# Optimization experiments

Hardware: AMD Instinct MI355X
Metric: run time of the kernel (lower is better)

## Reference

```python
import jax, jax.numpy as jnp
import numpy as np

D_MODEL = 1024
N_HEADS = 16
D_HEAD = D_MODEL // N_HEADS          # 64
FRACTION_TO_ROTATE = 0.25
ROT_DIM = int(FRACTION_TO_ROTATE * D_HEAD)  # 16 (even)
ROPE_BASE = 10000.0


def setup_inputs() -> dict:
    key = jax.random.key(0)
    ks = jax.random.split(key, 10)
    B, S = 2, 2048
    init = lambda k, fan_in, shape: jax.random.normal(k, shape, jnp.float32) / np.sqrt(fan_in)
    return {
        "x": jax.random.normal(ks[0], (B, S, D_MODEL), jnp.float32),
        "Wq": init(ks[1], D_MODEL, (D_MODEL, D_MODEL)),
        "bq": jnp.zeros((D_MODEL,), jnp.float32),
        "Wk": init(ks[2], D_MODEL, (D_MODEL, D_MODEL)),
        "bk": jnp.zeros((D_MODEL,), jnp.float32),
        "Wv": init(ks[3], D_MODEL, (D_MODEL, D_MODEL)),
        "bv": jnp.zeros((D_MODEL,), jnp.float32),
        "Wo": init(ks[4], D_MODEL, (D_MODEL, D_MODEL)),
        "bo": jnp.zeros((D_MODEL,), jnp.float32),
    }


def _apply_partial_rope(t, cos, sin):
    # t: [B, H, S, d_head]; rotate first ROT_DIM dims, pass the rest through.
    rot, rest = t[..., :ROT_DIM], t[..., ROT_DIM:]
    half = ROT_DIM // 2
    t1, t2 = rot[..., :half], rot[..., half:]
    # cos/sin: [S, half] -> broadcast over [B, H]
    r1 = t1 * cos - t2 * sin
    r2 = t1 * sin + t2 * cos
    return jnp.concatenate([r1, r2, rest], axis=-1)


def reference(x, Wq, bq, Wk, bk, Wv, bv, Wo, bo):
    B, S, D = x.shape
    q = (x @ Wq + bq).reshape(B, S, N_HEADS, D_HEAD).transpose(0, 2, 1, 3)
    k = (x @ Wk + bk).reshape(B, S, N_HEADS, D_HEAD).transpose(0, 2, 1, 3)
    v = (x @ Wv + bv).reshape(B, S, N_HEADS, D_HEAD).transpose(0, 2, 1, 3)

    half = ROT_DIM // 2
    inv_freq = 1.0 / (ROPE_BASE ** (jnp.arange(half, dtype=jnp.float32) / half))
    angles = jnp.arange(S, dtype=jnp.float32)[:, None] * inv_freq  # [S, half]
    cos, sin = jnp.cos(angles), jnp.sin(angles)

    q = _apply_partial_rope(q, cos, sin)
    k = _apply_partial_rope(k, cos, sin)

    scale = 1.0 / np.sqrt(D_HEAD).astype(np.float32)
    scores = jnp.einsum("bhqd,bhkd->bhqk", q, k) * scale  # [B,H,S,S]
    causal = jnp.tril(jnp.ones((S, S), dtype=bool))
    scores = jnp.where(causal, scores, jnp.finfo(scores.dtype).min)
    probs = jax.nn.softmax(scores, axis=-1)

    out = jnp.einsum("bhqk,bhkd->bhqd", probs, v)  # [B,H,S,d_head]
    out = out.transpose(0, 2, 1, 3).reshape(B, S, D)
    return out @ Wo + bo
```

## Files before the change

kernel.cpp:

```cpp
#include <hip/hip_runtime.h>
#include <hip/hip_bf16.h>
#include <math.h>

constexpr int DM = 1024;
constexpr int SEQ = 2048;
constexpr int BATCH = 2;
constexpr int NH = 16;
constexpr int DH = 64;
constexpr int MROWS = BATCH * SEQ;
constexpr float SCALE = 0.125f;

typedef __attribute__((ext_vector_type(8))) short short8;
typedef __attribute__((ext_vector_type(4))) float f32x4;
typedef unsigned short ushort_t;

__device__ __forceinline__ unsigned short f2b(float f) {
    __hip_bfloat16 h = __float2bfloat16(f);
    return __builtin_bit_cast(unsigned short, h);
}
__device__ __forceinline__ float b2f(unsigned short u) {
    unsigned int t = ((unsigned int)u) << 16;
    return __builtin_bit_cast(float, t);
}
__device__ __forceinline__ unsigned int cvtpk_bf16(float lo, float hi) {
    unsigned int r;
    asm("v_cvt_pk_bf16_f32 %0, %1, %2" : "=v"(r) : "v"(lo), "v"(hi));
    return r;
}
__device__ __forceinline__ f32x4 mfma16_bf16(uint2 a, uint2 b, f32x4 c) {
    asm volatile("v_mfma_f32_16x16x16_bf16 %0, %1, %2, %0"
                 : "+v"(c) : "v"(a), "v"(b));
    return c;
}

__device__ __forceinline__ void gload16(const ushort_t* g, ushort_t* l) {
    __builtin_amdgcn_global_load_lds(
        (const __attribute__((address_space(1))) void*)g,
        (__attribute__((address_space(3))) void*)l, 16, 0, 0);
}

__global__ __launch_bounds__(256) void conv_x(const float* __restrict__ x,
                                              ushort_t* __restrict__ xb) {
    const size_t idx = (size_t)blockIdx.x * 256 + threadIdx.x;
    const float4* src = (const float4*)(x + idx * 8);
    float4 a = src[0], b = src[1];
    short8 v;
    v[0] = (short)f2b(a.x); v[1] = (short)f2b(a.y);
    v[2] = (short)f2b(a.z); v[3] = (short)f2b(a.w);
    v[4] = (short)f2b(b.x); v[5] = (short)f2b(b.y);
    v[6] = (short)f2b(b.z); v[7] = (short)f2b(b.w);
    *(short8*)(xb + idx * 8) = v;
}

__global__ __launch_bounds__(256) void conv_w(
    const float* __restrict__ Wq, const float* __restrict__ Wk,
    const float* __restrict__ Wv, const float* __restrict__ Wo,
    ushort_t* __restrict__ Wqt, ushort_t* __restrict__ Wkt,
    ushort_t* __restrict__ Wvt, ushort_t* __restrict__ Wot) {
    const float* W; ushort_t* Wt;
    switch (blockIdx.z) {
        case 0:  W = Wq; Wt = Wqt; break;
        case 1:  W = Wk; Wt = Wkt; break;
        case 2:  W = Wv; Wt = Wvt; break;
        default: W = Wo; Wt = Wot; break;
    }
    __shared__ float L[64][65];
    const int n0 = blockIdx.x * 64, k0 = blockIdx.y * 64;
    const int t = threadIdx.x;
    const int tr = t >> 4, tc4 = (t & 15) * 4;
#pragma unroll
    for (int i = 0; i < 4; ++i) {
        int kk = tr + i * 16;
        float4 v = *(const float4*)&W[(size_t)(k0 + kk) * DM + n0 + tc4];
        L[kk][tc4 + 0] = v.x; L[kk][tc4 + 1] = v.y;
        L[kk][tc4 + 2] = v.z; L[kk][tc4 + 3] = v.w;
    }
    __syncthreads();
#pragma unroll
    for (int i = 0; i < 4; ++i) {
        int nn = tr + i * 16;
        ushort4 u;
        u.x = f2b(L[tc4 + 0][nn]); u.y = f2b(L[tc4 + 1][nn]);
        u.z = f2b(L[tc4 + 2][nn]); u.w = f2b(L[tc4 + 3][nn]);
        *(ushort4*)&Wt[(size_t)(n0 + nn) * DM + k0 + tc4] = u;
    }
}

#define BM 128
#define BN 128
#define BKK 32
#define NKT (DM / BKK)

__device__ __forceinline__ void stage_tile(const ushort_t* __restrict__ A,
                                           const ushort_t* __restrict__ B,
                                           int row0, int col0, int kt,
                                           ushort_t* As, ushort_t* Bs, int tid) {
#pragma unroll
    for (int i = 0; i < 2; ++i) {
        int f = i * 256 + tid;
        int r = f >> 2, c = (f & 3) ^ (r & 3);
        gload16(&A[(size_t)(row0 + r) * DM + kt * BKK + c * 8], &As[f * 8]);
        gload16(&B[(size_t)(col0 + r) * DM + kt * BKK + c * 8], &Bs[f * 8]);
    }
}

__device__ __forceinline__ void mfma_core(const ushort_t* __restrict__ A,
                                          const ushort_t* __restrict__ B,
                                          int row0, int col0,
                                          ushort_t* smem, f32x4 (&acc)[4][4]) {
    const int tid = threadIdx.x;
    const int wave = tid >> 6, lane = tid & 63;
    const int lg = lane >> 4, ln = lane & 15;
    const int wr = wave >> 1, wc = wave & 1;

    stage_tile(A, B, row0, col0, 0, smem, smem + 4096, tid);
    __syncthreads();

    int cur = 0;
    for (int kt = 0; kt < NKT; ++kt) {
        ushort_t* As = smem + cur * 8192;
        ushort_t* Bs = As + 4096;
        if (kt + 1 < NKT) {
            ushort_t* An = smem + (cur ^ 1) * 8192;
            stage_tile(A, B, row0, col0, kt + 1, An, An + 4096, tid);
        }

        short8 af[4], bf[4];
#pragma unroll
        for (int mi = 0; mi < 4; ++mi) {
            int r = wr * 64 + mi * 16 + ln;
            af[mi] = *(const short8*)&As[r * 32 + ((lg ^ (r & 3)) * 8)];
        }
#pragma unroll
        for (int ni = 0; ni < 4; ++ni) {
            int r = wc * 64 + ni * 16 + ln;
            bf[ni] = *(const short8*)&Bs[r * 32 + ((lg ^ (r & 3)) * 8)];
        }
        __builtin_amdgcn_s_setprio(1);
#pragma unroll
        for (int mi = 0; mi < 4; ++mi)
#pragma unroll
            for (int ni = 0; ni < 4; ++ni)
                acc[mi][ni] = __builtin_amdgcn_mfma_f32_16x16x32_bf16(
                    af[mi], bf[ni], acc[mi][ni], 0, 0, 0);
        __builtin_amdgcn_s_setprio(0);

        __syncthreads();
        cur ^= 1;
    }
}

__global__ __launch_bounds__(256) void mfma_gemm_qkv(
    const ushort_t* __restrict__ xb,
    const ushort_t* __restrict__ Wqt, const ushort_t* __restrict__ Wkt,
    const ushort_t* __restrict__ Wvt,
    const float* __restrict__ bq, const float* __restrict__ bk,
    const float* __restrict__ bv,
    ushort_t* __restrict__ qb, ushort_t* __restrict__ kb,
    ushort_t* __restrict__ vtb) {
    const ushort_t* W; const float* bias;
    if (blockIdx.z == 0)      { W = Wqt; bias = bq; }
    else if (blockIdx.z == 1) { W = Wkt; bias = bk; }
    else                      { W = Wvt; bias = bv; }

    const int row0 = blockIdx.y * BM;
    const int col0 = blockIdx.x * BN;
    __shared__ ushort_t smem[16384];
    f32x4 acc[4][4] = {};
    mfma_core(xb, W, row0, col0, smem, acc);

    const int tid = threadIdx.x;
    const int wave = tid >> 6, lane = tid & 63;
    const int lg = lane >> 4, ln = lane & 15;
    const int wr = wave >> 1, wc = wave & 1;
    const bool isV = (blockIdx.z == 2);

    __syncthreads();
    ushort_t* Cs = smem;
#pragma unroll
    for (int mi = 0; mi < 4; ++mi)
#pragma unroll
        for (int ni = 0; ni < 4; ++ni)
#pragma unroll
            for (int r = 0; r < 4; ++r) {
                int mrel = wr * 64 + mi * 16 + lg * 4 + r;
                int nrel = wc * 64 + ni * 16 + ln;
                float v = acc[mi][ni][r] + bias[col0 + nrel];
                Cs[isV ? (nrel * 128 + mrel) : (mrel * 128 + nrel)] = f2b(v);
            }
    __syncthreads();

    if (!isV) {
        ushort_t* out = (blockIdx.z == 0) ? qb : kb;
#pragma unroll
        for (int i = 0; i < 8; ++i) {
            int f = i * 256 + tid;
            int rrow = f >> 4, c8 = f & 15;
            int m = row0 + rrow;
            int b = m >> 11, s = m & (SEQ - 1);
            int n = col0 + c8 * 8;
            int h = n >> 6, d = n & 63;
            short8 val;
            if (d < 16) {
                const ushort_t* base = &Cs[rrow * 128 + (c8 & 8) * 8];
                const bool hi = (d >= 8);
#pragma unroll
                for (int j = 0; j < 8; ++j) {
                    float t1 = b2f(base[j]);
                    float t2 = b2f(base[8 + j]);
                    float invf = __expf(-(float)j * 1.1512925465f);
                    float ang = (float)s * invf;
                    float c_, si_;
                    __sincosf(ang, &si_, &c_);
                    val[j] = (short)f2b(hi ? (t1 * si_ + t2 * c_)
                                           : (t1 * c_ - t2 * si_));
                }
            } else {
                val = *(const short8*)&Cs[rrow * 128 + c8 * 8];
            }
            *(short8*)&out[((size_t)((b * NH + h) * SEQ) + s) * DH + d] = val;
        }
    } else {
#pragma unroll
        for (int i = 0; i < 8; ++i) {
            int f = i * 256 + tid;
            int nrow = f >> 4, c8 = f & 15;
            int n = col0 + nrow;
            int h = n >> 6, d = n & 63;
            int m = row0 + c8 * 8;
            int b = m >> 11, s = m & (SEQ - 1);
            *(short8*)&vtb[((size_t)((b * NH + h) * DH) + d) * SEQ + s] =
                *(const short8*)&Cs[nrow * 128 + c8 * 8];
        }
    }
}

__global__ __launch_bounds__(256) void mfma_gemm_out(
    const ushort_t* __restrict__ ctxb, const ushort_t* __restrict__ Wot,
    const float* __restrict__ bo, float* __restrict__ out) {
    const int row0 = blockIdx.y * BM;
    const int col0 = blockIdx.x * BN;
    __shared__ ushort_t smem[16384];
    f32x4 acc[4][4] = {};
    mfma_core(ctxb, Wot, row0, col0, smem, acc);

    const int tid = threadIdx.x;
    const int wave = tid >> 6, lane = tid & 63;
    const int lg = lane >> 4, ln = lane & 15;
    const int wr = wave >> 1, wc = wave & 1;
#pragma unroll
    for (int mi = 0; mi < 4; ++mi)
#pragma unroll
        for (int ni = 0; ni < 4; ++ni)
#pragma unroll
            for (int r = 0; r < 4; ++r) {
                int m = row0 + wr * 64 + mi * 16 + lg * 4 + r;
                int n = col0 + wc * 64 + ni * 16 + ln;
                out[(size_t)m * DM + n] = acc[mi][ni][r] + bo[n];
            }
}

#define AQT 64
#define AKT 64
#define NQT (SEQ / AQT)

__global__ __launch_bounds__(256) void attn_mfma(
    const ushort_t* __restrict__ qb, const ushort_t* __restrict__ kb,
    const ushort_t* __restrict__ vtb, ushort_t* __restrict__ ctxb) {
    constexpr float C1 = 0.18033688f;
    constexpr float M2 = 1.44269504f;
    const int bh = blockIdx.x;
    const int y = blockIdx.y;
    const int y0 = y & 7, g = y >> 3;
    const int qt = (g == 0) ? y0 : (g == 1) ? (15 - y0)
                 : (g == 2) ? (16 + y0) : (31 - y0);
    const int q0 = qt * AQT;

    const int tid = threadIdx.x;
    const int wave = tid >> 6;
    const int lane = tid & 63;
    const int lg = lane >> 4;
    const int ln = lane & 15;

    __shared__ ushort_t KT[2][64 * 64];
    __shared__ ushort_t VT[2][64 * 64];

    const ushort_t* kbase = kb + (size_t)bh * SEQ * DH;
    const ushort_t* vbase = vtb + (size_t)bh * DH * SEQ;
    const int b = bh >> 4, h = bh & 15;

    const ushort_t* qrow = qb + ((size_t)bh * SEQ + q0 + wave * 16 + ln) * DH;
    short8 qf0 = *(const short8*)&qrow[lg * 8];
    short8 qf1 = *(const short8*)&qrow[32 + lg * 8];

    f32x4 o[4];
#pragma unroll
    for (int nt = 0; nt < 4; nt++) o[nt] = f32x4{0.f, 0.f, 0.f, 0.f};
    float l = 0.f;

    const int ntiles = qt + 1;

#pragma unroll
    for (int i = 0; i < 2; i++) {
        int f = i * 256 + tid;
        int r = f >> 3, p = f & 7, c = p ^ (r & 7);
        gload16(&kbase[(size_t)r * DH + c * 8], &KT[0][f * 8]);
        gload16(&vbase[(size_t)r * SEQ + c * 8], &VT[0][f * 8]);
    }

    int cur = 0;
    for (int t = 0; t < ntiles; ++t) {
        __syncthreads();

        if (t + 1 < ntiles) {
            const int nb0 = (t + 1) * AKT;
            const int nxt = cur ^ 1;
#pragma unroll
            for (int i = 0; i < 2; i++) {
                int f = i * 256 + tid;
                int r = f >> 3, p = f & 7, c = p ^ (r & 7);
                gload16(&kbase[(size_t)(nb0 + r) * DH + c * 8], &KT[nxt][f * 8]);
                gload16(&vbase[(size_t)r * SEQ + nb0 + c * 8], &VT[nxt][f * 8]);
            }
        }

        float st[4][4];
        __builtin_amdgcn_s_setprio(1);
#pragma unroll
        for (int kt = 0; kt < 4; kt++) {
            f32x4 acc = f32x4{0.f, 0.f, 0.f, 0.f};
            int krow = kt * 16 + ln;
            short8 b0 = *(const short8*)&KT[cur][krow * 64 + ((lg ^ (krow & 7)) * 8)];
            short8 b1 = *(const short8*)&KT[cur][krow * 64 + (((4 + lg) ^ (krow & 7)) * 8)];
            acc = __builtin_amdgcn_mfma_f32_16x16x32_bf16(b0, qf0, acc, 0, 0, 0);
            acc = __builtin_amdgcn_mfma_f32_16x16x32_bf16(b1, qf1, acc, 0, 0, 0);
#pragma unroll
            for (int r = 0; r < 4; r++) st[kt][r] = acc[r];
        }
        __builtin_amdgcn_s_setprio(0);

        if (t == ntiles - 1) {
            const int qrel = wave * 16 + ln;
#pragma unroll
            for (int kt = 0; kt < 4; kt++)
#pragma unroll
                for (int r = 0; r < 4; r++)
                    if (kt * 16 + lg * 4 + r > qrel) st[kt][r] = -1e30f;
        }

        uint2 pkq[4];
#pragma unroll
        for (int kt = 0; kt < 4; kt++) {
            float pv[4];
#pragma unroll
            for (int r = 0; r < 4; r++) {
                pv[r] = exp2f(fmaf(C1, st[kt][r], -M2));
                l += pv[r];
            }
            pkq[kt].x = cvtpk_bf16(pv[0], pv[1]);
            pkq[kt].y = cvtpk_bf16(pv[2], pv[3]);
        }

        __builtin_amdgcn_s_setprio(1);
#pragma unroll
        for (int nt = 0; nt < 4; nt++) {
            int vrow = nt * 16 + ln;
#pragma unroll
            for (int kt = 0; kt < 4; kt++) {
                int chunk = (2 * kt + (lg >> 1)) ^ (vrow & 7);
                uint2 vb = *(const uint2*)&VT[cur][vrow * 64 + chunk * 8 + (lg & 1) * 4];
                o[nt] = mfma16_bf16(pkq[kt], vb, o[nt]);
            }
        }
        __builtin_amdgcn_s_setprio(0);

        cur ^= 1;
    }

    l += __shfl_xor(l, 16);
    l += __shfl_xor(l, 32);
    const float rcp = 1.f / l;
#pragma unroll
    for (int r = 0; r < 4; r++) {
        float invl = __shfl(rcp, (lane & 48) | (lg * 4 + r));
        int qg = q0 + wave * 16 + lg * 4 + r;
        ushort_t* op = ctxb + ((size_t)(b * SEQ + qg)) * DM + h * DH;
#pragma unroll
        for (int nt = 0; nt < 4; nt++)
            op[nt * 16 + ln] = f2b(o[nt][r] * invl);
    }
}

extern "C" void kernel_launch(void* const* d_in, const int* in_sizes, int n_in,
                              void* d_out, int out_size, void* d_ws, size_t ws_size,
                              hipStream_t stream) {
    const float* x  = (const float*)d_in[0];
    const float* Wq = (const float*)d_in[1];
    const float* bq = (const float*)d_in[2];
    const float* Wk = (const float*)d_in[3];
    const float* bk = (const float*)d_in[4];
    const float* Wv = (const float*)d_in[5];
    const float* bv = (const float*)d_in[6];
    const float* Wo = (const float*)d_in[7];
    const float* bo = (const float*)d_in[8];
    float* out = (float*)d_out;

    constexpr size_t TSZ = (size_t)MROWS * DM;
    constexpr size_t WSZ = (size_t)DM * DM;
    ushort_t* xb  = (ushort_t*)d_ws;
    ushort_t* Wqt = xb + TSZ;
    ushort_t* Wkt = Wqt + WSZ;
    ushort_t* Wvt = Wkt + WSZ;
    ushort_t* Wot = Wvt + WSZ;
    ushort_t* qbp = Wot + WSZ;
    ushort_t* kbp = qbp + TSZ;
    ushort_t* vtp = kbp + TSZ;
    ushort_t* ctxb = vtp + TSZ;

    conv_x<<<TSZ / 8 / 256, 256, 0, stream>>>(x, xb);
    conv_w<<<dim3(16, 16, 4), 256, 0, stream>>>(Wq, Wk, Wv, Wo, Wqt, Wkt, Wvt, Wot);

    mfma_gemm_qkv<<<dim3(DM / BN, MROWS / BM, 3), 256, 0, stream>>>(
        xb, Wqt, Wkt, Wvt, bq, bk, bv, qbp, kbp, vtp);

    attn_mfma<<<dim3(BATCH * NH, NQT), 256, 0, stream>>>(qbp, kbp, vtp, ctxb);

    mfma_gemm_out<<<dim3(DM / BN, MROWS / BM), 256, 0, stream>>>(ctxb, Wot, bo, out);
}
```

Baseline: 120.8 us.

## Split long causal attention query tiles into two KV chunks with a reduce kernel

Query tiles 16-31 are split into two blocks, one covering KV tiles 0-15 and one covering the rest, so long causal rows no longer sit on a single block. Each split writes unnormalized bf16 partial outputs and row sums into reused workspace, and a new reduce kernel adds them and normalizes. This is meant to balance work across blocks and cut the tail of the attention grid. The cost is an extra launch, extra memory traffic and bf16 rounding of the partials. The asm volatile on the MFMA is also dropped so the compiler can schedule it more freely.

```diff
diff --git a/kernel.cpp b/kernel.cpp
--- a/kernel.cpp
+++ b/kernel.cpp
@@ -28,8 +28,8 @@
     return r;
 }
 __device__ __forceinline__ f32x4 mfma16_bf16(uint2 a, uint2 b, f32x4 c) {
-    asm volatile("v_mfma_f32_16x16x16_bf16 %0, %1, %2, %0"
-                 : "+v"(c) : "v"(a), "v"(b));
+    asm("v_mfma_f32_16x16x16_bf16 %0, %1, %2, %0"
+        : "+v"(c) : "v"(a), "v"(b));
     return c;
 }
 
@@ -266,14 +266,17 @@
 
 __global__ __launch_bounds__(256) void attn_mfma(
     const ushort_t* __restrict__ qb, const ushort_t* __restrict__ kb,
-    const ushort_t* __restrict__ vtb, ushort_t* __restrict__ ctxb) {
+    const ushort_t* __restrict__ vtb, ushort_t* __restrict__ ctxb,
+    ushort_t* __restrict__ opart, float* __restrict__ lpart) {
     constexpr float C1 = 0.18033688f;
     constexpr float M2 = 1.44269504f;
     const int bh = blockIdx.x;
     const int y = blockIdx.y;
-    const int y0 = y & 7, g = y >> 3;
-    const int qt = (g == 0) ? y0 : (g == 1) ? (15 - y0)
-                 : (g == 2) ? (16 + y0) : (31 - y0);
+
+    int qt, t0, t1, chunk;
+    if (y < 16)      { qt = 16 + y;  t0 = 0;  t1 = 16;     chunk = 0; }
+    else if (y < 32) { qt = 47 - y;  t0 = 16; t1 = qt + 1; chunk = 1; }
+    else             { qt = 47 - y;  t0 = 0;  t1 = qt + 1; chunk = -1; }
     const int q0 = qt * AQT;
 
     const int tid = threadIdx.x;
@@ -298,21 +301,19 @@
     for (int nt = 0; nt < 4; nt++) o[nt] = f32x4{0.f, 0.f, 0.f, 0.f};
     float l = 0.f;
 
-    const int ntiles = qt + 1;
-
 #pragma unroll
     for (int i = 0; i < 2; i++) {
         int f = i * 256 + tid;
         int r = f >> 3, p = f & 7, c = p ^ (r & 7);
-        gload16(&kbase[(size_t)r * DH + c * 8], &KT[0][f * 8]);
-        gload16(&vbase[(size_t)r * SEQ + c * 8], &VT[0][f * 8]);
+        gload16(&kbase[(size_t)(t0 * AKT + r) * DH + c * 8], &KT[0][f * 8]);
+        gload16(&vbase[(size_t)r * SEQ + t0 * AKT + c * 8], &VT[0][f * 8]);
     }
 
     int cur = 0;
-    for (int t = 0; t < ntiles; ++t) {
+    for (int t = t0; t < t1; ++t) {
         __syncthreads();
 
-        if (t + 1 < ntiles) {
+        if (t + 1 < t1) {
             const int nb0 = (t + 1) * AKT;
             const int nxt = cur ^ 1;
 #pragma unroll
@@ -339,7 +340,7 @@
         }
         __builtin_amdgcn_s_setprio(0);
 
-        if (t == ntiles - 1) {
+        if (t == qt) {
             const int qrel = wave * 16 + ln;
 #pragma unroll
             for (int kt = 0; kt < 4; kt++)
@@ -367,8 +368,8 @@
             int vrow = nt * 16 + ln;
 #pragma unroll
             for (int kt = 0; kt < 4; kt++) {
-                int chunk = (2 * kt + (lg >> 1)) ^ (vrow & 7);
-                uint2 vb = *(const uint2*)&VT[cur][vrow * 64 + chunk * 8 + (lg & 1) * 4];
+                int chunk16 = (2 * kt + (lg >> 1)) ^ (vrow & 7);
+                uint2 vb = *(const uint2*)&VT[cur][vrow * 64 + chunk16 * 8 + (lg & 1) * 4];
                 o[nt] = mfma16_bf16(pkq[kt], vb, o[nt]);
             }
         }
@@ -379,15 +380,58 @@
 
     l += __shfl_xor(l, 16);
     l += __shfl_xor(l, 32);
-    const float rcp = 1.f / l;
-#pragma unroll
-    for (int r = 0; r < 4; r++) {
-        float invl = __shfl(rcp, (lane & 48) | (lg * 4 + r));
-        int qg = q0 + wave * 16 + lg * 4 + r;
-        ushort_t* op = ctxb + ((size_t)(b * SEQ + qg)) * DM + h * DH;
-#pragma unroll
-        for (int nt = 0; nt < 4; nt++)
-            op[nt * 16 + ln] = f2b(o[nt][r] * invl);
+
+    if (chunk >= 0) {
+        const int pid = ((bh << 4) + (qt - 16)) * 2 + chunk;
+        if (lg == 0) lpart[pid * 64 + wave * 16 + ln] = l;
+        ushort_t* ob = opart + (size_t)pid * 4096;
+#pragma unroll
+        for (int r = 0; r < 4; r++) {
+            int qrel = wave * 16 + lg * 4 + r;
+#pragma unroll
+            for (int nt = 0; nt < 4; nt++)
+                ob[qrel * 64 + nt * 16 + ln] = f2b(o[nt][r]);
+        }
+    } else {
+        const float rcp = 1.f / l;
+#pragma unroll
+        for (int r = 0; r < 4; r++) {
+            float invl = __shfl(rcp, (lane & 48) | (lg * 4 + r));
+            int qg = q0 + wave * 16 + lg * 4 + r;
+            ushort_t* op = ctxb + ((size_t)(b * SEQ + qg)) * DM + h * DH;
+#pragma unroll
+            for (int nt = 0; nt < 4; nt++)
+                op[nt * 16 + ln] = f2b(o[nt][r] * invl);
+        }
+    }
+}
+
+__global__ __launch_bounds__(256) void attn_reduce(
+    const ushort_t* __restrict__ opart, const float* __restrict__ lpart,
+    ushort_t* __restrict__ ctxb) {
+    const int bh = blockIdx.x;
+    const int qt = 16 + blockIdx.y;
+    const int tid = threadIdx.x;
+    const int q = tid >> 2;
+    const int d0 = (tid & 3) * 16;
+
+    const int pid0 = ((bh << 4) + (qt - 16)) * 2;
+    const ushort_t* o0 = opart + (size_t)pid0 * 4096 + q * 64 + d0;
+    const ushort_t* o1 = opart + (size_t)(pid0 + 1) * 4096 + q * 64 + d0;
+    const float inv = 1.f / (lpart[pid0 * 64 + q] + lpart[(pid0 + 1) * 64 + q]);
+
+    const int b = bh >> 4, h = bh & 15;
+    ushort_t* op = ctxb + ((size_t)(b * SEQ + qt * 64 + q)) * DM + h * DH + d0;
+#pragma unroll
+    for (int half = 0; half < 2; ++half) {
+        short8 a = *(const short8*)&o0[half * 8];
+        short8 c = *(const short8*)&o1[half * 8];
+        short8 r;
+#pragma unroll
+        for (int j = 0; j < 8; ++j)
+            r[j] = (short)f2b((b2f((unsigned short)a[j]) +
+                               b2f((unsigned short)c[j])) * inv);
+        *(short8*)&op[half * 8] = r;
     }
 }
 
@@ -417,13 +461,18 @@
     ushort_t* vtp = kbp + TSZ;
     ushort_t* ctxb = vtp + TSZ;
 
+    ushort_t* opart = xb;
+    float* lpart = (float*)Wqt;
+
     conv_x<<<TSZ / 8 / 256, 256, 0, stream>>>(x, xb);
     conv_w<<<dim3(16, 16, 4), 256, 0, stream>>>(Wq, Wk, Wv, Wo, Wqt, Wkt, Wvt, Wot);
 
     mfma_gemm_qkv<<<dim3(DM / BN, MROWS / BM, 3), 256, 0, stream>>>(
         xb, Wqt, Wkt, Wvt, bq, bk, bv, qbp, kbp, vtp);
 
-    attn_mfma<<<dim3(BATCH * NH, NQT), 256, 0, stream>>>(qbp, kbp, vtp, ctxb);
+    attn_mfma<<<dim3(BATCH * NH, 48), 256, 0, stream>>>(
+        qbp, kbp, vtp, ctxb, opart, lpart);
+    attn_reduce<<<dim3(BATCH * NH, 16), 256, 0, stream>>>(opart, lpart, ctxb);
 
     mfma_gemm_out<<<dim3(DM / BN, MROWS / BM), 256, 0, stream>>>(ctxb, Wot, bo, out);
 }
```

Result: faster. 117.5 us (-2.7%).
